# Performance work log

Measured on AMD Instinct MI355X. Metric: run time of the kernel, lower is better.

The kernel has to match this reference:

```python
import jax, jax.numpy as jnp
import numpy as np

ALPHA = 0.2  # LeakyReLU negative slope
NEG_INF = -9e15


def setup_inputs() -> dict:
    key = jax.random.key(0)
    ks = jax.random.split(key, 6)
    B, N, F_in, F_out = 16, 1024, 1024, 512
    x = jax.random.normal(ks[0], (B, N, F_in), dtype=jnp.float32)
    adj = jax.random.randint(ks[1], (B, N, N), 0, 2, dtype=jnp.int32)
    W = jax.random.normal(ks[2], (F_in, F_out), dtype=jnp.float32) * 0.02
    a = jax.random.normal(ks[3], (2 * F_out, 1), dtype=jnp.float32) * 0.02
    fc_w = jax.random.normal(ks[4], (F_out, 2 * F_out), dtype=jnp.float32) * 0.02
    fc_b = jnp.zeros((F_out,), dtype=jnp.float32)
    return {"x": x, "adj": adj, "W": W, "a": a, "fc_w": fc_w, "fc_b": fc_b}


def reference(x, adj, W, a, fc_w, fc_b):
    # h: [B, N, F_out]
    h = jnp.matmul(x, W)
    F_out = W.shape[1]
    # The original builds a_input = concat(h_i, h_j) of shape [B,N,N,2F] and
    # contracts with a. Equivalently (same math, no O(N^2 F) intermediate):
    # e_ij = leakyrelu(h_i . a[:F] + h_j . a[F:])
    a1 = a[:F_out, 0]  # [F_out]
    a2 = a[F_out:, 0]  # [F_out]
    f1 = jnp.einsum('bnf,f->bn', h, a1)  # source term
    f2 = jnp.einsum('bnf,f->bn', h, a2)  # target term
    e = jax.nn.leaky_relu(f1[:, :, None] + f2[:, None, :], negative_slope=ALPHA)  # [B,N,N]
    attention = jnp.where(adj > 0, e, jnp.full_like(e, NEG_INF))
    attention = jax.nn.softmax(attention, axis=2)
    # dropout is identity in eval mode
    agg = jnp.matmul(attention, h)  # [B,N,F_out]
    h_prime = jnp.concatenate([agg, h], axis=2)  # [B,N,2F]
    h_prime = jnp.matmul(h_prime, fc_w.T) + fc_b
    return jax.nn.elu(h_prime)  # concat=True path
```

## Files before the change

### kernel.cpp

```cpp
#include <hip/hip_runtime.h>

#define ALPHA 0.2f

typedef __attribute__((ext_vector_type(8))) short short8;
typedef __attribute__((ext_vector_type(4))) float f32x4;

__device__ __forceinline__ unsigned short f2b(float f) {
  unsigned int u; __builtin_memcpy(&u, &f, 4);
  unsigned int r = (u + 0x7FFFu + ((u >> 16) & 1u)) >> 16;
  return (unsigned short)r;
}
__device__ __forceinline__ float b2f(unsigned short v) {
  unsigned int u = ((unsigned int)v) << 16; float f; __builtin_memcpy(&f, &u, 4); return f;
}
__device__ __forceinline__ void gl_lds16(const unsigned short* g, unsigned short* l) {
  __builtin_amdgcn_global_load_lds((__attribute__((address_space(1))) void*)g,
                                   (__attribute__((address_space(3))) void*)l, 16, 0, 0);
}
__device__ __forceinline__ uint4 pack8(float4 v0, float4 v1) {
  alignas(16) unsigned short o[8];
  o[0] = f2b(v0.x); o[1] = f2b(v0.y); o[2] = f2b(v0.z); o[3] = f2b(v0.w);
  o[4] = f2b(v1.x); o[5] = f2b(v1.y); o[6] = f2b(v1.z); o[7] = f2b(v1.w);
  return *(const uint4*)o;
}

__device__ __forceinline__ void cvt_f4(const float* __restrict__ in,
                                       unsigned short* __restrict__ out,
                                       unsigned int f4idx) {
  float4 v = ((const float4*)in)[f4idx];
  alignas(8) unsigned short o[4];
  o[0] = f2b(v.x); o[1] = f2b(v.y); o[2] = f2b(v.z); o[3] = f2b(v.w);
  ((uint2*)out)[f4idx] = *(const uint2*)o;
}

__global__ __launch_bounds__(256) void prep1(const float* __restrict__ fcw,
                                             unsigned short* __restrict__ fcwb,
                                             const float* __restrict__ W,
                                             unsigned short* __restrict__ Wt) {
  __shared__ alignas(16) unsigned short tile[64][72];
  unsigned int bx = blockIdx.x;
  unsigned int tid = threadIdx.x;
  if (bx < 256u) {
    unsigned int base = bx * 512u;
    cvt_f4(fcw, fcwb, base + tid);
    cvt_f4(fcw, fcwb, base + 256u + tid);
  } else {
    unsigned int idx = bx - 256u;
    unsigned int k0 = (idx >> 3) * 64, n0 = (idx & 7) * 64;
    #pragma unroll
    for (int p = 0; p < 4; p++) {
      int r = p * 16 + (tid >> 4);
      int c = (tid & 15) * 4;
      float4 v = *(const float4*)(W + (size_t)(k0 + r) * 512 + n0 + c);
      tile[r][c] = f2b(v.x); tile[r][c + 1] = f2b(v.y);
      tile[r][c + 2] = f2b(v.z); tile[r][c + 3] = f2b(v.w);
    }
    __syncthreads();
    int f = tid >> 2;
    int ic = (tid & 3) * 16;
    alignas(16) unsigned short buf[16];
    #pragma unroll
    for (int k = 0; k < 16; k++) buf[k] = tile[ic + k][f];
    uint4* dst = (uint4*)(Wt + (size_t)(n0 + f) * 1024 + k0 + ic);
    dst[0] = ((const uint4*)buf)[0];
    dst[1] = ((const uint4*)buf)[1];
  }
}

__global__ __launch_bounds__(256) void prep2(const unsigned short* __restrict__ hp,
                                             const float* __restrict__ a,
                                             float* __restrict__ f1, float* __restrict__ f2,
                                             unsigned short* __restrict__ ht) {
  __shared__ alignas(16) unsigned short tile[64][72];
  int bx = blockIdx.x;
  int tid = threadIdx.x;
  if (bx < 4096) {
    int row = bx * 4 + (tid >> 6);
    int lane = tid & 63;
    const unsigned short* hrow = hp + (size_t)row * 1024 + 512;
    uint4 raw = *(const uint4*)(hrow + lane * 8);
    alignas(16) unsigned short hv[8]; __builtin_memcpy(hv, &raw, 16);
    float s1 = 0.f, s2 = 0.f;
    #pragma unroll
    for (int j = 0; j < 8; j++) {
      float hf = b2f(hv[j]);
      s1 += hf * a[lane * 8 + j];
      s2 += hf * a[512 + lane * 8 + j];
    }
    #pragma unroll
    for (int o = 32; o > 0; o >>= 1) { s1 += __shfl_down(s1, o); s2 += __shfl_down(s2, o); }
    if (lane == 0) { f1[row] = s1; f2[row] = s2; }
  } else {
    int idx = bx - 4096;
    int b = idx >> 7;
    int f0 = ((idx >> 4) & 7) * 64;
    int i0 = (idx & 15) * 64;
    #pragma unroll
    for (int p = 0; p < 2; p++) {
      int r = p * 32 + (tid >> 3);
      int c = (tid & 7) * 8;
      uint4 v = *(const uint4*)(hp + (size_t)(b * 1024 + i0 + r) * 1024 + 512 + f0 + c);
      *(uint4*)(&tile[r][c]) = v;
    }
    __syncthreads();
    int f = tid >> 2;
    int ic = (tid & 3) * 16;
    alignas(16) unsigned short buf[16];
    #pragma unroll
    for (int k = 0; k < 16; k++) buf[k] = tile[ic + k][f];
    uint4* dst = (uint4*)(ht + (size_t)(b * 512 + f0 + f) * 1024 + i0 + ic);
    dst[0] = ((const uint4*)buf)[0];
    dst[1] = ((const uint4*)buf)[1];
  }
}

__global__ __launch_bounds__(256) void rowsum_P(const int* __restrict__ adj,
                                                const float* __restrict__ f1,
                                                const float* __restrict__ f2,
                                                float* __restrict__ invl,
                                                unsigned short* __restrict__ P) {
  int row = blockIdx.x * 4 + (threadIdx.x >> 6);
  int lane = threadIdx.x & 63;
  int b = row >> 10;
  float f1v = f1[row];
  const int4* ap = (const int4*)(adj + (size_t)row * 1024) + lane * 4;
  int4 a0 = ap[0];
  int4 a1 = ap[1];
  int4 a2 = ap[2];
  int4 a3 = ap[3];
  int av[16] = {a0.x, a0.y, a0.z, a0.w, a1.x, a1.y, a1.z, a1.w,
                a2.x, a2.y, a2.z, a2.w, a3.x, a3.y, a3.z, a3.w};
  const float* f2p = f2 + (b << 10) + lane * 16;
  float4 v0 = ((const float4*)f2p)[0];
  float4 v1 = ((const float4*)f2p)[1];
  float4 v2 = ((const float4*)f2p)[2];
  float4 v3 = ((const float4*)f2p)[3];
  float fv[16] = {v0.x, v0.y, v0.z, v0.w, v1.x, v1.y, v1.z, v1.w,
                  v2.x, v2.y, v2.z, v2.w, v3.x, v3.y, v3.z, v3.w};
  float s = 0.f;
  alignas(16) unsigned short o[16];
  #pragma unroll
  for (int j = 0; j < 16; j++) {
    float p = 0.f;
    if (av[j] > 0) {
      float z = f1v + fv[j];
      z = z > 0.f ? z : ALPHA * z;
      p = __expf(z);
      s += p;
    }
    o[j] = f2b(p);
  }
  uint4* dst = (uint4*)(P + (size_t)row * 1024 + lane * 16);
  dst[0] = ((const uint4*)o)[0];
  dst[1] = ((const uint4*)o)[1];
  #pragma unroll
  for (int off = 32; off > 0; off >>= 1) s += __shfl_down(s, off);
  if (lane == 0) invl[row] = 1.0f / s;
}

template <int EPI, int CVTA>
__global__ __launch_bounds__(512, 4) void gemm_bt(
    const void* __restrict__ A_, size_t aBS,
    const unsigned short* __restrict__ Bt, size_t bBS,
    int K,
    void* __restrict__ outp, size_t oBS, int ldo, int ocol,
    const float* __restrict__ scale,
    const float* __restrict__ bias) {
  __shared__ alignas(16) unsigned short As[2 * 128 * 64];
  __shared__ alignas(16) unsigned short Bs[2 * 128 * 64];
  const int tid = threadIdx.x;
  const int lane = tid & 63;
  const int w = tid >> 6;
  const int m0 = blockIdx.x * 128;
  const int n0 = blockIdx.y * 128;
  const int zb = blockIdx.z;
  const unsigned short* Btb = Bt + (size_t)zb * bBS;

  f32x4 acc[4][2];
  #pragma unroll
  for (int i = 0; i < 4; i++)
    #pragma unroll
    for (int j = 0; j < 2; j++)
      #pragma unroll
      for (int r = 0; r < 4; r++) acc[i][j][r] = 0.f;

  const int lr = lane >> 3;
  const int lc = (lane & 7) ^ (lr & 7);
  const unsigned short* ag = nullptr;
  const float* agf = nullptr;
  if (CVTA)
    agf = (const float*)A_ + (size_t)zb * aBS + (size_t)(m0 + w * 8 + lr) * K + lc * 8;
  else
    ag = (const unsigned short*)A_ + (size_t)zb * aBS + (size_t)(m0 + w * 8 + lr) * K + lc * 8;
  const unsigned short* bg = Btb + (size_t)(n0 + w * 8 + lr) * K + lc * 8;
  const int sb0 = (w * 8) * 64;
  const int sb1 = (64 + w * 8) * 64;
  const int lofs = lane * 8;

  const int wm = (w & 1) * 64;
  const int wn = (w >> 1) * 32;
  const int row16 = lane & 15;
  const int quad = lane >> 4;
  const int sw = row16 & 7;

  if (CVTA) {
    float4 av[2][2];
    #pragma unroll
    for (int t = 0; t < 2; t++) {
      av[t][0] = *(const float4*)(agf + (size_t)(t * 64) * K);
      av[t][1] = *(const float4*)(agf + (size_t)(t * 64) * K + 4);
    }
    gl_lds16(bg, Bs + sb0);
    gl_lds16(bg + (size_t)64 * K, Bs + sb1);
    *(uint4*)(As + sb0 + lofs) = pack8(av[0][0], av[0][1]);
    *(uint4*)(As + sb1 + lofs) = pack8(av[1][0], av[1][1]);
  } else {
    gl_lds16(ag, As + sb0);
    gl_lds16(ag + (size_t)64 * K, As + sb1);
    gl_lds16(bg, Bs + sb0);
    gl_lds16(bg + (size_t)64 * K, Bs + sb1);
  }
  __syncthreads();

  int bufo = 0;
  for (int k0 = 0; k0 < K; k0 += 64) {
    const int nbufo = bufo ^ 8192;
    const bool pf = (k0 + 64 < K);
    float4 av[2][2];
    if (pf) {
      if (CVTA) {
        #pragma unroll
        for (int t = 0; t < 2; t++) {
          av[t][0] = *(const float4*)(agf + (k0 + 64) + (size_t)(t * 64) * K);
          av[t][1] = *(const float4*)(agf + (k0 + 64) + (size_t)(t * 64) * K + 4);
        }
      } else {
        gl_lds16(ag + (k0 + 64), As + nbufo + sb0);
        gl_lds16(ag + (k0 + 64) + (size_t)64 * K, As + nbufo + sb1);
      }
      gl_lds16(bg + (k0 + 64), Bs + nbufo + sb0);
      gl_lds16(bg + (k0 + 64) + (size_t)64 * K, Bs + nbufo + sb1);
    }
    short8 af[2][4], bf[2][2];
    #pragma unroll
    for (int s = 0; s < 2; s++) {
      #pragma unroll
      for (int i = 0; i < 4; i++)
        af[s][i] = *(const short8*)(As + bufo + (wm + i * 16 + row16) * 64 + ((s * 4 + quad) ^ sw) * 8);
      #pragma unroll
      for (int j = 0; j < 2; j++)
        bf[s][j] = *(const short8*)(Bs + bufo + (wn + j * 16 + row16) * 64 + ((s * 4 + quad) ^ sw) * 8);
    }
    #pragma unroll
    for (int s = 0; s < 2; s++)
      #pragma unroll
      for (int am = 0; am < 4; am++)
        #pragma unroll
        for (int bn = 0; bn < 2; bn++)
          acc[am][bn] = __builtin_amdgcn_mfma_f32_16x16x32_bf16(af[s][am], bf[s][bn], acc[am][bn], 0, 0, 0);
    if (pf && CVTA) {
      *(uint4*)(As + nbufo + sb0 + lofs) = pack8(av[0][0], av[0][1]);
      *(uint4*)(As + nbufo + sb1 + lofs) = pack8(av[1][0], av[1][1]);
    }
    __syncthreads();
    bufo = nbufo;
  }

  const int col = lane & 15;
  const int r0 = quad * 4;
  #pragma unroll
  for (int am = 0; am < 4; am++) {
    #pragma unroll
    for (int bn = 0; bn < 2; bn++) {
      #pragma unroll
      for (int r = 0; r < 4; r++) {
        int m = m0 + wm + am * 16 + r0 + r;
        int n = n0 + wn + bn * 16 + col;
        float v = acc[am][bn][r];
        if (EPI == 3) v *= scale[zb * 1024 + m];
        if (EPI == 2) {
          v += bias[n];
          v = v > 0.f ? v : expm1f(v);
          ((float*)outp)[(size_t)m * ldo + n] = v;
        } else {
          ((unsigned short*)outp)[(size_t)zb * oBS + (size_t)m * ldo + ocol + n] = f2b(v);
        }
      }
    }
  }
}

extern "C" void kernel_launch(void* const* d_in, const int* in_sizes, int n_in,
                              void* d_out, int out_size, void* d_ws, size_t ws_size,
                              hipStream_t stream) {
  const float* x   = (const float*)d_in[0];
  const int*   adj = (const int*)d_in[1];
  const float* W   = (const float*)d_in[2];
  const float* a   = (const float*)d_in[3];
  const float* fcw = (const float*)d_in[4];
  const float* fcb = (const float*)d_in[5];
  float* out = (float*)d_out;
  char* ws = (char*)d_ws;

  unsigned short* P    = (unsigned short*)(ws);
  unsigned short* hp   = (unsigned short*)(ws + 33554432);
  unsigned short* ht   = (unsigned short*)(ws + 67108864);
  unsigned short* Wt   = (unsigned short*)(ws + 83886080);
  unsigned short* fcwb = (unsigned short*)(ws + 84934656);
  float* f1            = (float*)(ws + 85983232);
  float* f2            = (float*)(ws + 86048768);
  float* invl          = (float*)(ws + 86114304);

  prep1<<<384, 256, 0, stream>>>(fcw, fcwb, W, Wt);

  gemm_bt<1, 1><<<dim3(128, 4, 1), 512, 0, stream>>>(x, 0, Wt, 0, 1024,
                                                     hp, 0, 1024, 512, nullptr, nullptr);
  prep2<<<6144, 256, 0, stream>>>(hp, a, f1, f2, ht);
  rowsum_P<<<4096, 256, 0, stream>>>(adj, f1, f2, invl, P);

  gemm_bt<3, 0><<<dim3(8, 4, 16), 512, 0, stream>>>(P, 1024 * 1024, ht, 512 * 1024, 1024,
                                                    hp, 1024 * 1024, 1024, 0, invl, nullptr);
  gemm_bt<2, 0><<<dim3(128, 4, 1), 512, 0, stream>>>(hp, 0, fcwb, 0, 1024,
                                                     out, 0, 512, 0, nullptr, fcb);
}
```

Baseline: 251.7 us.

## Deepen GEMM prefetch to two stages with explicit vmcnt waits

Restructures the bf16 MFMA GEMM main loop so that global loads for tile k+2 are issued into the buffer just consumed, right after its fragments are read into registers. Fine-grained s_waitcnt vmcnt counts replace full __syncthreads, so later loads stay in flight while earlier ones are consumed. For the fp32-A conversion path, two register stages of A values are carried. The aim is to hide global memory latency behind the MFMA work. The cost is more registers and reliance on exact vmcnt accounting, which is fragile if the compiler reorders or adds memory operations.

```diff
diff --git a/kernel.cpp b/kernel.cpp
--- a/kernel.cpp
+++ b/kernel.cpp
@@ -23,6 +23,10 @@
   o[4] = f2b(v1.x); o[5] = f2b(v1.y); o[6] = f2b(v1.z); o[7] = f2b(v1.w);
   return *(const uint4*)o;
 }
+__device__ __forceinline__ void vm6() { asm volatile("s_waitcnt vmcnt(6)" ::: "memory"); }
+__device__ __forceinline__ void vm4() { asm volatile("s_waitcnt vmcnt(4)" ::: "memory"); }
+__device__ __forceinline__ void vm0() { asm volatile("s_waitcnt vmcnt(0)" ::: "memory"); }
+__device__ __forceinline__ void lg0() { asm volatile("s_waitcnt lgkmcnt(0)" ::: "memory"); }
 
 __device__ __forceinline__ void cvt_f4(const float* __restrict__ in,
                                        unsigned short* __restrict__ out,
@@ -203,54 +207,77 @@
   const int quad = lane >> 4;
   const int sw = row16 & 7;
 
+  const int nk = K >> 6;
+  float4 avc[2][2], avn[2][2];
+
   if (CVTA) {
-    float4 av[2][2];
+    float4 av0[2][2];
     #pragma unroll
     for (int t = 0; t < 2; t++) {
-      av[t][0] = *(const float4*)(agf + (size_t)(t * 64) * K);
-      av[t][1] = *(const float4*)(agf + (size_t)(t * 64) * K + 4);
+      av0[t][0] = *(const float4*)(agf + (size_t)(t * 64) * K);
+      av0[t][1] = *(const float4*)(agf + (size_t)(t * 64) * K + 4);
     }
     gl_lds16(bg, Bs + sb0);
     gl_lds16(bg + (size_t)64 * K, Bs + sb1);
-    *(uint4*)(As + sb0 + lofs) = pack8(av[0][0], av[0][1]);
-    *(uint4*)(As + sb1 + lofs) = pack8(av[1][0], av[1][1]);
+    #pragma unroll
+    for (int t = 0; t < 2; t++) {
+      avc[t][0] = *(const float4*)(agf + 64 + (size_t)(t * 64) * K);
+      avc[t][1] = *(const float4*)(agf + 64 + (size_t)(t * 64) * K + 4);
+    }
+    gl_lds16(bg + 64, Bs + 8192 + sb0);
+    gl_lds16(bg + 64 + (size_t)64 * K, Bs + 8192 + sb1);
+    vm6();
+    *(uint4*)(As + sb0 + lofs) = pack8(av0[0][0], av0[0][1]);
+    *(uint4*)(As + sb1 + lofs) = pack8(av0[1][0], av0[1][1]);
   } else {
     gl_lds16(ag, As + sb0);
     gl_lds16(ag + (size_t)64 * K, As + sb1);
     gl_lds16(bg, Bs + sb0);
     gl_lds16(bg + (size_t)64 * K, Bs + sb1);
-  }
-  __syncthreads();
+    gl_lds16(ag + 64, As + 8192 + sb0);
+    gl_lds16(ag + 64 + (size_t)64 * K, As + 8192 + sb1);
+    gl_lds16(bg + 64, Bs + 8192 + sb0);
+    gl_lds16(bg + 64 + (size_t)64 * K, Bs + 8192 + sb1);
+    vm4();
+  }
+  lg0();
+  __builtin_amdgcn_s_barrier();
 
   int bufo = 0;
-  for (int k0 = 0; k0 < K; k0 += 64) {
+  for (int k = 0; k < nk; k++) {
     const int nbufo = bufo ^ 8192;
-    const bool pf = (k0 + 64 < K);
-    float4 av[2][2];
-    if (pf) {
+    const bool st2 = (k + 2 < nk);
+    const bool pub = (k + 1 < nk);
+
+    short8 af[2][4], bf[2][2];
+    #pragma unroll
+    for (int s = 0; s < 2; s++) {
+      #pragma unroll
+      for (int i = 0; i < 4; i++)
+        af[s][i] = *(const short8*)(As + bufo + (wm + i * 16 + row16) * 64 + ((s * 4 + quad) ^ sw) * 8);
+      #pragma unroll
+      for (int j = 0; j < 2; j++)
+        bf[s][j] = *(const short8*)(Bs + bufo + (wn + j * 16 + row16) * 64 + ((s * 4 + quad) ^ sw) * 8);
+    }
+    lg0();
+    __builtin_amdgcn_s_barrier();
+
+    if (st2) {
+      const int ko = (k + 2) * 64;
       if (CVTA) {
         #pragma unroll
         for (int t = 0; t < 2; t++) {
-          av[t][0] = *(const float4*)(agf + (k0 + 64) + (size_t)(t * 64) * K);
-          av[t][1] = *(const float4*)(agf + (k0 + 64) + (size_t)(t * 64) * K + 4);
+          avn[t][0] = *(const float4*)(agf + ko + (size_t)(t * 64) * K);
+          avn[t][1] = *(const float4*)(agf + ko + (size_t)(t * 64) * K + 4);
         }
       } else {
-        gl_lds16(ag + (k0 + 64), As + nbufo + sb0);
-        gl_lds16(ag + (k0 + 64) + (size_t)64 * K, As + nbufo + sb1);
+        gl_lds16(ag + ko, As + bufo + sb0);
+        gl_lds16(ag + ko + (size_t)64 * K, As + bufo + sb1);
       }
-      gl_lds16(bg + (k0 + 64), Bs + nbufo + sb0);
-      gl_lds16(bg + (k0 + 64) + (size_t)64 * K, Bs + nbufo + sb1);
-    }
-    short8 af[2][4], bf[2][2];
-    #pragma unroll
-    for (int s = 0; s < 2; s++) {
-      #pragma unroll
-      for (int i = 0; i < 4; i++)
-        af[s][i] = *(const short8*)(As + bufo + (wm + i * 16 + row16) * 64 + ((s * 4 + quad) ^ sw) * 8);
-      #pragma unroll
-      for (int j = 0; j < 2; j++)
-        bf[s][j] = *(const short8*)(Bs + bufo + (wn + j * 16 + row16) * 64 + ((s * 4 + quad) ^ sw) * 8);
-    }
+      gl_lds16(bg + ko, Bs + bufo + sb0);
+      gl_lds16(bg + ko + (size_t)64 * K, Bs + bufo + sb1);
+    }
+
     #pragma unroll
     for (int s = 0; s < 2; s++)
       #pragma unroll
@@ -258,11 +285,20 @@
         #pragma unroll
         for (int bn = 0; bn < 2; bn++)
           acc[am][bn] = __builtin_amdgcn_mfma_f32_16x16x32_bf16(af[s][am], bf[s][bn], acc[am][bn], 0, 0, 0);
-    if (pf && CVTA) {
-      *(uint4*)(As + nbufo + sb0 + lofs) = pack8(av[0][0], av[0][1]);
-      *(uint4*)(As + nbufo + sb1 + lofs) = pack8(av[1][0], av[1][1]);
-    }
-    __syncthreads();
+
+    if (pub) {
+      if (CVTA) {
+        if (st2) vm6(); else vm0();
+        *(uint4*)(As + nbufo + sb0 + lofs) = pack8(avc[0][0], avc[0][1]);
+        *(uint4*)(As + nbufo + sb1 + lofs) = pack8(avc[1][0], avc[1][1]);
+        #pragma unroll
+        for (int t = 0; t < 2; t++) { avc[t][0] = avn[t][0]; avc[t][1] = avn[t][1]; }
+        lg0();
+      } else {
+        if (st2) vm4(); else vm0();
+      }
+      __builtin_amdgcn_s_barrier();
+    }
     bufo = nbufo;
   }
 
```

Measured after the change: 254.6 us. About the same (+1.2%).
